# Optimization experiments

Measured on AMD Instinct MI355X. Metric: run time of the kernel, lower is better.

## Reference

```python
import jax, jax.numpy as jnp
import numpy as np

N = 6144
M_VID = 1024
M_AUD = 128
APPERTURE = 20
EPS = 1e-6


def setup_inputs() -> dict:
    key = jax.random.key(0)
    ks = jax.random.split(key, 16)
    s = 0.02
    inp = {
        "x": jax.random.normal(ks[0], (1, N, M_VID), dtype=jnp.float32),
        "x_audio": jax.random.normal(ks[1], (1, N, M_AUD), dtype=jnp.float32),
        "seq_len": N,
        "audio_len": N,
        # video self-attention (torch Linear convention: W is [out, in])
        "Wk_v": jax.random.normal(ks[2], (M_VID, M_VID), dtype=jnp.float32) * s,
        "Wq_v": jax.random.normal(ks[3], (M_VID, M_VID), dtype=jnp.float32) * s,
        "Wv_v": jax.random.normal(ks[4], (M_VID, M_VID), dtype=jnp.float32) * s,
        "Wo_v": jax.random.normal(ks[5], (M_VID, M_VID), dtype=jnp.float32) * s,
        # audio self-attention
        "Wk_a": jax.random.normal(ks[6], (M_AUD, M_AUD), dtype=jnp.float32) * s,
        "Wq_a": jax.random.normal(ks[7], (M_AUD, M_AUD), dtype=jnp.float32) * s,
        "Wv_a": jax.random.normal(ks[8], (M_AUD, M_AUD), dtype=jnp.float32) * s,
        "Wo_a": jax.random.normal(ks[9], (M_AUD, M_AUD), dtype=jnp.float32) * s,
        # MLP head
        "ka_w": jax.random.normal(ks[10], (1024, M_VID + M_AUD), dtype=jnp.float32) * s,
        "ka_b": jnp.zeros((1024,), dtype=jnp.float32),
        "kd_w": jax.random.normal(ks[11], (1, 1024), dtype=jnp.float32) * s,
        "kd_b": jnp.zeros((1,), dtype=jnp.float32),
        # layer norms
        "ln_y_g": jnp.ones((M_VID,), dtype=jnp.float32),
        "ln_y_b": jnp.zeros((M_VID,), dtype=jnp.float32),
        "ln_ya_g": jnp.ones((M_AUD,), dtype=jnp.float32),
        "ln_ya_b": jnp.zeros((M_AUD,), dtype=jnp.float32),
        "ln_ka_g": jnp.ones((1024,), dtype=jnp.float32),
        "ln_ka_b": jnp.zeros((1024,), dtype=jnp.float32),
    }
    return inp


def _layer_norm(x, g, b):
    mu = jnp.mean(x, axis=-1, keepdims=True)
    var = jnp.mean((x - mu) ** 2, axis=-1, keepdims=True)
    return (x - mu) / jnp.sqrt(var + EPS) * g + b


def _self_attention(x, Wk, Wq, Wv, Wo):
    # x: [N, d]
    n = x.shape[0]
    K = x @ Wk.T
    Q = (x @ Wq.T) * 0.06
    V = x @ Wv.T
    logits = Q @ K.T  # [N, N]
    # keep only |i-j| < apperture (trimask masks |i-j| >= apperture)
    idx = jnp.arange(n)
    band = jnp.abs(idx[:, None] - idx[None, :]) < APPERTURE
    logits = jnp.where(band, logits, -jnp.inf)
    att = jax.nn.softmax(logits, axis=-1)  # [N, N]
    # torch: y = (V^T @ att)^T == att^T @ V  (note the transpose on att!)
    y = att.T @ V
    return y @ Wo.T, att


def reference(x, x_audio, seq_len, audio_len,
              Wk_v, Wq_v, Wv_v, Wo_v,
              Wk_a, Wq_a, Wv_a, Wo_a,
              ka_w, ka_b, kd_w, kd_b,
              ln_y_g, ln_y_b, ln_ya_g, ln_ya_b, ln_ka_g, ln_ka_b):
    m = x.shape[2]
    m_audio = x_audio.shape[2]
    xf = x.reshape(-1, m)            # [N, 1024]
    xa = x_audio.reshape(-1, m_audio)  # [N, 128]

    y, att_w = _self_attention(xf, Wk_v, Wq_v, Wv_v, Wo_v)
    y = _layer_norm(y + xf, ln_y_g, ln_y_b)

    ya, att_wa = _self_attention(xa, Wk_a, Wq_a, Wv_a, Wo_a)
    ya = _layer_norm(ya + xa, ln_ya_g, ln_ya_b)

    y_comb = jnp.concatenate((y, ya), axis=1)        # [N, 1152]
    att_comb = jnp.concatenate((att_w, att_wa), axis=1)  # [N, 2N]

    h = jax.nn.relu(y_comb @ ka_w.T + ka_b)
    h = _layer_norm(h, ln_ka_g, ln_ka_b)
    score = jax.nn.sigmoid(h @ kd_w.T + kd_b)  # [N, 1]
    score = score.reshape(1, -1)               # [1, N]
    return score, att_comb
```

## Files before the change

kernel.cpp:

```cpp
#include <hip/hip_runtime.h>
#include <stdint.h>

typedef unsigned short u16;
typedef unsigned int u32;
typedef __attribute__((ext_vector_type(8))) short bf16x8;
typedef __attribute__((ext_vector_type(4))) short s16x4;
typedef __attribute__((ext_vector_type(4))) float f32x4;
typedef __attribute__((ext_vector_type(2))) float f32x2;

#define DEV __device__ __forceinline__

DEV u16 f2bf(float f) {
  union { float f; unsigned u; } v; v.f = f;
  unsigned r = v.u + 0x7fffu + ((v.u >> 16) & 1u);
  return (u16)(r >> 16);
}
DEV float bf2f(u16 h) {
  union { u32 u; float f; } v; v.u = ((u32)h) << 16; return v.f;
}
DEV float lo16(u32 w) { union { u32 u; float f; } v; v.u = w << 16; return v.f; }
DEV float hi16(u32 w) { union { u32 u; float f; } v; v.u = w & 0xFFFF0000u; return v.f; }
DEV int imax(int a, int b) { return a > b ? a : b; }
DEV int imin(int a, int b) { return a < b ? a : b; }

DEV int xcd_swz(int b0, int nwg) {
  int q = nwg >> 3, r = nwg & 7, x = b0 & 7, l = b0 >> 3;
  return (x < r ? x * (q + 1) : r * (q + 1) + (x - r) * q) + l;
}

DEV void g2lds16(const u16* g, u16* l) {
  __builtin_amdgcn_global_load_lds(
      (const __attribute__((address_space(1))) void*)g,
      (__attribute__((address_space(3))) void*)l, 16, 0, 0);
}

#define NSEG 5
struct CastTab {
  const float* src[NSEG];
  u16* dst[NSEG];
  int start[NSEG + 1];
};
struct TransTab {
  const float* src[6];
  u16* dst[6];
  int n[6];
  int start[7];
};

__global__ __launch_bounds__(256) void vas_prep(CastTab t, int total4,
                                                int castBlocks, TransTab tt) {
  if ((int)blockIdx.x < castBlocks) {
    int idx = blockIdx.x * 256 + threadIdx.x;
    if (idx >= total4) return;
    int s = 0;
#pragma unroll
    for (int k = 1; k < NSEG; ++k)
      if (idx >= t.start[k]) s = k;
    int local = idx - t.start[s];
    f32x4 f = ((const f32x4*)t.src[s])[local];
    s16x4 o;
    o.x = (short)f2bf(f.x);
    o.y = (short)f2bf(f.y);
    o.z = (short)f2bf(f.z);
    o.w = (short)f2bf(f.w);
    ((s16x4*)t.dst[s])[local] = o;
  } else {
    __shared__ float tl[32][33];
    int b = blockIdx.x - castBlocks;
    int s = 0;
#pragma unroll
    for (int k = 1; k < 6; ++k)
      if (b >= tt.start[k]) s = k;
    b -= tt.start[s];
    const float* src = tt.src[s];
    u16* dst = tt.dst[s];
    const int n = tt.n[s];
    const int tpr = n >> 5;
    const int tr = (b / tpr) * 32, tc = (b % tpr) * 32;
    const int lx = threadIdx.x & 31, ly = threadIdx.x >> 5;
#pragma unroll
    for (int r = 0; r < 4; ++r)
      tl[ly + r * 8][lx] = src[(size_t)(tr + ly + r * 8) * n + tc + lx];
    __syncthreads();
#pragma unroll
    for (int r = 0; r < 4; ++r)
      dst[(size_t)(tc + ly + r * 8) * n + tr + lx] = f2bf(tl[lx][ly + r * 8]);
  }
}

struct GemmP {
  const u16* A;
  const u16* W;
  void* C;
  const float* bias;
  int M, Nn, K, mode;
};

__global__ __launch_bounds__(256) void vas_gemm4(
    GemmP p0, GemmP p1, GemmP p2, GemmP p3, int s1, int s2, int s3) {
  const int bs = xcd_swz(blockIdx.x, gridDim.x);

  GemmP p;
  int bid;
  if (bs < s1) { p = p0; bid = bs; }
  else if (bs < s2) { p = p1; bid = bs - s1; }
  else if (bs < s3) { p = p2; bid = bs - s2; }
  else { p = p3; bid = bs - s3; }

  __shared__ u16 As[2][128 * 32];
  __shared__ u16 Ws[2][128 * 32];
  const int tid = threadIdx.x;
  const int lane = tid & 63;
  const int wave = tid >> 6;

  const int Mb = p.M >> 7, Nb = p.Nn >> 7;
  const int GM = 8;
  int per = GM * Nb;
  int g = bid / per;
  int rem = bid - g * per;
  int gm = imin(GM, Mb - g * GM);
  int mblk = g * GM + rem % gm;
  int nblk = rem / gm;
  const int m0 = mblk * 128;
  const int n0 = nblk * 128;
  const int wm = (wave >> 1) * 64;
  const int wn = (wave & 1) * 64;

  const int smat = wave >> 1;
  const int skh = wave & 1;
  const u16* ssrc = smat ? p.W : p.A;
  const int sbase = smat ? n0 : m0;
  u16* sdstBase = (smat ? &Ws[skh][0] : &As[skh][0]) + lane * 8;
  const int srow = lane >> 2;
  const int scol = (lane & 3) * 8;

  f32x4 acc[4][4] = {};

  for (int k0 = 0; k0 < p.K; k0 += 64) {
#pragma unroll
    for (int u = 0; u < 8; ++u) {
      int r0 = u * 16;
      g2lds16(ssrc + (size_t)(sbase + r0 + srow) * p.K + (k0 + skh * 32 + scol),
              sdstBase + r0 * 32);
    }
    __syncthreads();
#pragma unroll
    for (int kk = 0; kk < 2; ++kk) {
      bf16x8 af[4], bfr[4];
#pragma unroll
      for (int t = 0; t < 4; ++t)
        af[t] = *(const bf16x8*)(&As[kk][0] + (wm + t * 16 + (lane & 15)) * 32 + (lane >> 4) * 8);
#pragma unroll
      for (int t = 0; t < 4; ++t)
        bfr[t] = *(const bf16x8*)(&Ws[kk][0] + (wn + t * 16 + (lane & 15)) * 32 + (lane >> 4) * 8);
#pragma unroll
      for (int mi = 0; mi < 4; ++mi)
#pragma unroll
        for (int ni = 0; ni < 4; ++ni)
          acc[mi][ni] = __builtin_amdgcn_mfma_f32_16x16x32_bf16(af[mi], bfr[ni], acc[mi][ni], 0, 0, 0);
    }
    __syncthreads();
  }

#pragma unroll
  for (int mi = 0; mi < 4; ++mi) {
#pragma unroll
    for (int ni = 0; ni < 4; ++ni) {
      int col = n0 + wn + ni * 16 + (lane & 15);
      float bv = p.bias ? p.bias[col] : 0.f;
#pragma unroll
      for (int r = 0; r < 4; ++r) {
        int row = m0 + wm + mi * 16 + (lane >> 4) * 4 + r;
        float vv = acc[mi][ni][r] + bv;
        size_t idx = (size_t)row * p.Nn + col;
        if (p.mode == 0) ((float*)p.C)[idx] = vv;
        else if (p.mode == 1) ((u16*)p.C)[idx] = f2bf(fmaxf(vv, 0.f));
        else ((u16*)p.C)[idx] = f2bf(vv);
      }
    }
  }
}

__global__ __launch_bounds__(256) void vas_gemmh(
    GemmP p, const float* __restrict__ kw, const float* __restrict__ gw,
    float* __restrict__ part) {
  const int bid = xcd_swz(blockIdx.x, gridDim.x);

  __shared__ u16 As[2][128 * 32];
  __shared__ u16 Ws[2][128 * 32];
  __shared__ float hp[2][128][3];
  const int tid = threadIdx.x;
  const int lane = tid & 63;
  const int wave = tid >> 6;

  const int Mb = p.M >> 7, Nb = p.Nn >> 7;
  const int GM = 8;
  int per = GM * Nb;
  int g = bid / per;
  int rem = bid - g * per;
  int gm = imin(GM, Mb - g * GM);
  int mblk = g * GM + rem % gm;
  int nblk = rem / gm;
  const int m0 = mblk * 128;
  const int n0 = nblk * 128;
  const int wm = (wave >> 1) * 64;
  const int wn = (wave & 1) * 64;

  const int smat = wave >> 1;
  const int skh = wave & 1;
  const u16* ssrc = smat ? p.W : p.A;
  const int sbase = smat ? n0 : m0;
  u16* sdstBase = (smat ? &Ws[skh][0] : &As[skh][0]) + lane * 8;
  const int srow = lane >> 2;
  const int scol = (lane & 3) * 8;

  f32x4 acc[4][4] = {};

  for (int k0 = 0; k0 < p.K; k0 += 64) {
#pragma unroll
    for (int u = 0; u < 8; ++u) {
      int r0 = u * 16;
      g2lds16(ssrc + (size_t)(sbase + r0 + srow) * p.K + (k0 + skh * 32 + scol),
              sdstBase + r0 * 32);
    }
    __syncthreads();
#pragma unroll
    for (int kk = 0; kk < 2; ++kk) {
      bf16x8 af[4], bfr[4];
#pragma unroll
      for (int t = 0; t < 4; ++t)
        af[t] = *(const bf16x8*)(&As[kk][0] + (wm + t * 16 + (lane & 15)) * 32 + (lane >> 4) * 8);
#pragma unroll
      for (int t = 0; t < 4; ++t)
        bfr[t] = *(const bf16x8*)(&Ws[kk][0] + (wn + t * 16 + (lane & 15)) * 32 + (lane >> 4) * 8);
#pragma unroll
      for (int mi = 0; mi < 4; ++mi)
#pragma unroll
        for (int ni = 0; ni < 4; ++ni)
          acc[mi][ni] = __builtin_amdgcn_mfma_f32_16x16x32_bf16(af[mi], bfr[ni], acc[mi][ni], 0, 0, 0);
    }
    __syncthreads();
  }

  float kwg[4], bb[4];
#pragma unroll
  for (int ni = 0; ni < 4; ++ni) {
    int col = n0 + wn + ni * 16 + (lane & 15);
    kwg[ni] = kw[col] * gw[col];
    bb[ni] = p.bias ? p.bias[col] : 0.f;
  }
#pragma unroll
  for (int mi = 0; mi < 4; ++mi) {
#pragma unroll
    for (int r = 0; r < 4; ++r) {
      float s1 = 0.f, s2 = 0.f, dd = 0.f;
#pragma unroll
      for (int ni = 0; ni < 4; ++ni) {
        float vv = fmaxf(acc[mi][ni][r] + bb[ni], 0.f);
        s1 += vv;
        s2 += vv * vv;
        dd += vv * kwg[ni];
      }
#pragma unroll
      for (int off = 1; off < 16; off <<= 1) {
        s1 += __shfl_xor(s1, off);
        s2 += __shfl_xor(s2, off);
        dd += __shfl_xor(dd, off);
      }
      if ((lane & 15) == 0) {
        int row = wm + mi * 16 + (lane >> 4) * 4 + r;
        hp[wave & 1][row][0] = s1;
        hp[wave & 1][row][1] = s2;
        hp[wave & 1][row][2] = dd;
      }
    }
  }
  __syncthreads();
  if (tid < 128) {
    float* pp = part + ((size_t)(m0 + tid) * 8 + nblk) * 3;
    pp[0] = hp[0][tid][0] + hp[1][tid][0];
    pp[1] = hp[0][tid][1] + hp[1][tid][1];
    pp[2] = hp[0][tid][2] + hp[1][tid][2];
  }
}

__global__ __launch_bounds__(256) void vas_score(
    const float* __restrict__ part, const float* __restrict__ kw,
    const float* __restrict__ g, const float* __restrict__ b,
    const float* __restrict__ kb, float* __restrict__ score, int N) {
  const int tid = threadIdx.x, lane = tid & 63, wave = tid >> 6;
  __shared__ float shc[2][4];
  f32x4 kv = ((const f32x4*)kw)[tid];
  f32x4 gv = ((const f32x4*)g)[tid];
  f32x4 bv = ((const f32x4*)b)[tid];
  float c1 = kv.x * gv.x + kv.y * gv.y + kv.z * gv.z + kv.w * gv.w;
  float c2 = kv.x * bv.x + kv.y * bv.y + kv.z * bv.z + kv.w * bv.w;
#pragma unroll
  for (int off = 32; off; off >>= 1) {
    c1 += __shfl_xor(c1, off);
    c2 += __shfl_xor(c2, off);
  }
  if (lane == 0) { shc[0][wave] = c1; shc[1][wave] = c2; }
  __syncthreads();
  float C1 = shc[0][0] + shc[0][1] + shc[0][2] + shc[0][3];
  float C2 = shc[1][0] + shc[1][1] + shc[1][2] + shc[1][3];
  int row = blockIdx.x * 256 + tid;
  if (row < N) {
    const float* pp = part + (size_t)row * 24;
    float s1 = 0.f, s2 = 0.f, dd = 0.f;
#pragma unroll
    for (int k = 0; k < 8; ++k) {
      s1 += pp[k * 3];
      s2 += pp[k * 3 + 1];
      dd += pp[k * 3 + 2];
    }
    float mu = s1 / 1024.f;
    float var = s2 / 1024.f - mu * mu;
    float inv = rsqrtf(var + 1e-6f);
    float P = inv * dd - inv * mu * C1 + C2 + kb[0];
    score[row] = 1.f / (1.f + __expf(-P));
  }
}

__global__ __launch_bounds__(256) void vas_battn(
    const u16* __restrict__ Xv, const u16* __restrict__ Xa,
    const u16* __restrict__ KKVv, const u16* __restrict__ KKVa,
    float* __restrict__ bandV, float* __restrict__ bandA,
    float* __restrict__ attBase, int N, float scale, int vb) {
  const int lane = threadIdx.x & 63;
  const int wave = threadIdx.x >> 6;
  const bool video = blockIdx.x < (u32)vb;
  const int i = (video ? blockIdx.x : blockIdx.x - vb) * 4 + wave;
  const int lo = imax(i - 19, 0);
  const int hi = imin(i + 19, N - 1);
  const int nj = hi - lo + 1;
  float logit = 0.f;
  __shared__ float a_sh[4][40];

  if (video) {
    float qf[16];
    const u16* qrow = Xv + (size_t)i * 1024;
#pragma unroll
    for (int c = 0; c < 2; ++c) {
      bf16x8 qv = *(const bf16x8*)(qrow + c * 512 + lane * 8);
      const u32* qw = (const u32*)&qv;
#pragma unroll
      for (int t = 0; t < 4; ++t) {
        qf[c * 8 + 2 * t] = lo16(qw[t]);
        qf[c * 8 + 2 * t + 1] = hi16(qw[t]);
      }
    }
#pragma unroll 2
    for (int s = 0; s < nj; ++s) {
      const u16* kr = KKVv + (size_t)(lo + s) * 2048;
      float p = 0.f;
#pragma unroll
      for (int c = 0; c < 2; ++c) {
        bf16x8 kv = *(const bf16x8*)(kr + c * 512 + lane * 8);
        const u32* kw = (const u32*)&kv;
#pragma unroll
        for (int t = 0; t < 4; ++t)
          p += lo16(kw[t]) * qf[c * 8 + 2 * t] + hi16(kw[t]) * qf[c * 8 + 2 * t + 1];
      }
#pragma unroll
      for (int off = 32; off; off >>= 1) p += __shfl_xor(p, off);
      if (lane == s) logit = p;
    }
  } else {
    u32 q = *(const u32*)(Xa + (size_t)i * 128 + lane * 2);
    float q0 = lo16(q), q1 = hi16(q);
#pragma unroll 2
    for (int s = 0; s < nj; ++s) {
      u32 k = *(const u32*)(KKVa + (size_t)(lo + s) * 256 + lane * 2);
      float p = lo16(k) * q0 + hi16(k) * q1;
#pragma unroll
      for (int off = 32; off; off >>= 1) p += __shfl_xor(p, off);
      if (lane == s) logit = p;
    }
  }

  logit *= scale;
  float v = (lane < nj) ? logit : -3.4e38f;
  float mx = v;
#pragma unroll
  for (int off = 32; off; off >>= 1) mx = fmaxf(mx, __shfl_xor(mx, off));
  float e = (lane < nj) ? __expf(v - mx) : 0.f;
  float den = e;
#pragma unroll
  for (int off = 32; off; off >>= 1) den += __shfl_xor(den, off);
  float att = (lane < nj) ? e / den : 0.f;
  float* band = video ? bandV : bandA;
  if (lane < 40) {
    band[i * 40 + lane] = att;
    a_sh[wave][lane] = att;
  }

  f32x4* rowp = (f32x4*)(attBase + (size_t)i * 2 * N + (video ? 0 : N));
  const int nchunks = N / 4;
  const int cLo = lo >> 2, cHi = hi >> 2;
  for (int c = lane; c < nchunks; c += 64) {
    f32x4 o = {0.f, 0.f, 0.f, 0.f};
    if (c >= cLo && c <= cHi) {
      int col0 = c * 4;
#pragma unroll
      for (int e2 = 0; e2 < 4; ++e2) {
        int col = col0 + e2;
        if (col >= lo && col <= hi) o[e2] = a_sh[wave][col - lo];
      }
    }
    __builtin_nontemporal_store(o, &rowp[c]);
  }
}

#define JT 8
__global__ __launch_bounds__(256) void vas_apply_ln(
    const u16* __restrict__ KKVv, const u16* __restrict__ KKVa,
    const float* __restrict__ bandV, const float* __restrict__ bandA,
    const float* __restrict__ Xv, const float* __restrict__ Xa,
    const float* __restrict__ gv, const float* __restrict__ bv_,
    const float* __restrict__ ga, const float* __restrict__ ba,
    u16* __restrict__ out, int outStride, int N, int vb) {
  const int tid = threadIdx.x;
  __shared__ float a_sh[(JT + 38) * JT];
  __shared__ float red[2][JT][4];

  if (blockIdx.x < (u32)vb) {
    const int j0 = blockIdx.x * JT;
    const int base = j0 - 19;
    for (int idx = tid; idx < (JT + 38) * JT; idx += 256) {
      int s = idx / JT, jj = idx % JT;
      int i = base + s;
      int j = j0 + jj;
      float w = 0.f;
      if (i >= 0 && i < N) {
        int d = j - i;
        if (d > -20 && d < 20) w = bandV[i * 40 + (j - imax(i - 19, 0))];
      }
      a_sh[s * JT + jj] = w;
    }
    __syncthreads();

    f32x4 acc[JT] = {};
    const int sLo = imax(0, -base);
    const int sHi = imin(JT + 38, N - base);
    s16x4 nxt = *(const s16x4*)(KKVv + (size_t)(base + sLo) * 2048 + 1024 + tid * 4);
    for (int s = sLo; s < sHi; ++s) {
      s16x4 raw = nxt;
      if (s + 1 < sHi)
        nxt = *(const s16x4*)(KKVv + (size_t)(base + s + 1) * 2048 + 1024 + tid * 4);
      f32x4 vv;
      vv.x = bf2f((u16)raw.x);
      vv.y = bf2f((u16)raw.y);
      vv.z = bf2f((u16)raw.z);
      vv.w = bf2f((u16)raw.w);
#pragma unroll
      for (int jj = 0; jj < JT; ++jj) {
        float a = a_sh[s * JT + jj];
        acc[jj].x += a * vv.x;
        acc[jj].y += a * vv.y;
        acc[jj].z += a * vv.z;
        acc[jj].w += a * vv.w;
      }
    }

    const int lane = tid & 63, wave = tid >> 6;
#pragma unroll
    for (int jj = 0; jj < JT; ++jj) {
      f32x4 x4 = ((const f32x4*)(Xv + (size_t)(j0 + jj) * 1024))[tid];
      f32x4 v;
      v.x = acc[jj].x + x4.x;
      v.y = acc[jj].y + x4.y;
      v.z = acc[jj].z + x4.z;
      v.w = acc[jj].w + x4.w;
      acc[jj] = v;
      float s = v.x + v.y + v.z + v.w;
      float s2 = v.x * v.x + v.y * v.y + v.z * v.z + v.w * v.w;
#pragma unroll
      for (int off = 32; off; off >>= 1) {
        s += __shfl_xor(s, off);
        s2 += __shfl_xor(s2, off);
      }
      if (lane == 0) { red[0][jj][wave] = s; red[1][jj][wave] = s2; }
    }
    __syncthreads();
    f32x4 gg = ((const f32x4*)gv)[tid];
    f32x4 bb = ((const f32x4*)bv_)[tid];
#pragma unroll
    for (int jj = 0; jj < JT; ++jj) {
      float S = red[0][jj][0] + red[0][jj][1] + red[0][jj][2] + red[0][jj][3];
      float S2 = red[1][jj][0] + red[1][jj][1] + red[1][jj][2] + red[1][jj][3];
      float mu = S / 1024.f;
      float var = S2 / 1024.f - mu * mu;
      float inv = rsqrtf(var + 1e-6f);
      f32x4 v = acc[jj];
      s16x4 o;
      o.x = (short)f2bf((v.x - mu) * inv * gg.x + bb.x);
      o.y = (short)f2bf((v.y - mu) * inv * gg.y + bb.y);
      o.z = (short)f2bf((v.z - mu) * inv * gg.z + bb.z);
      o.w = (short)f2bf((v.w - mu) * inv * gg.w + bb.w);
      *(s16x4*)(out + (size_t)(j0 + jj) * outStride + tid * 4) = o;
    }
  } else {
    const int lane = tid & 63;
    const int wave = tid >> 6;
    const int j = (blockIdx.x - vb) * 4 + wave;
    const int lo = imax(j - 19, 0);
    const int hi = imin(j + 19, N - 1);
    const int ni = hi - lo + 1;
    float* aw = a_sh + wave * 40;
    if (lane < ni) {
      int i = lo + lane;
      aw[lane] = bandA[i * 40 + (j - imax(i - 19, 0))];
    }
    __syncthreads();
    f32x2 acc = {0.f, 0.f};
#pragma unroll 4
    for (int s = 0; s < ni; ++s) {
      float a = aw[s];
      u32 k = *(const u32*)(KKVa + (size_t)(lo + s) * 256 + 128 + lane * 2);
      acc.x += a * lo16(k);
      acc.y += a * hi16(k);
    }
    f32x2 x2 = *(const f32x2*)(Xa + (size_t)j * 128 + lane * 2);
    float vx = acc.x + x2.x;
    float vy = acc.y + x2.y;
    float s = vx + vy, s2 = vx * vx + vy * vy;
#pragma unroll
    for (int off = 32; off; off >>= 1) {
      s += __shfl_xor(s, off);
      s2 += __shfl_xor(s2, off);
    }
    float mu = s / 128.f;
    float var = s2 / 128.f - mu * mu;
    float inv = rsqrtf(var + 1e-6f);
    f32x2 g2 = *(const f32x2*)(ga + lane * 2);
    f32x2 b2 = *(const f32x2*)(ba + lane * 2);
    u32 o = (u32)f2bf((vx - mu) * inv * g2.x + b2.x) |
            ((u32)f2bf((vy - mu) * inv * g2.y + b2.y) << 16);
    *(u32*)(out + (size_t)j * outStride + 1024 + lane * 2) = o;
  }
}

extern "C" void kernel_launch(void* const* d_in, const int* in_sizes, int n_in,
                              void* d_out, int out_size, void* d_ws, size_t ws_size,
                              hipStream_t stream) {
  const float* x = (const float*)d_in[0];
  const float* xa = (const float*)d_in[1];
  const float* Wk_v = (const float*)d_in[4];
  const float* Wq_v = (const float*)d_in[5];
  const float* Wv_v = (const float*)d_in[6];
  const float* Wo_v = (const float*)d_in[7];
  const float* Wk_a = (const float*)d_in[8];
  const float* Wq_a = (const float*)d_in[9];
  const float* Wv_a = (const float*)d_in[10];
  const float* Wo_a = (const float*)d_in[11];
  const float* ka_w = (const float*)d_in[12];
  const float* ka_b = (const float*)d_in[13];
  const float* kd_w = (const float*)d_in[14];
  const float* kd_b = (const float*)d_in[15];
  const float* ln_y_g = (const float*)d_in[16];
  const float* ln_y_b = (const float*)d_in[17];
  const float* ln_ya_g = (const float*)d_in[18];
  const float* ln_ya_b = (const float*)d_in[19];
  const float* ln_ka_g = (const float*)d_in[20];
  const float* ln_ka_b = (const float*)d_in[21];

  const int N = in_sizes[0] / 1024;
  const int MV = 1024, MA = 128, MH = 1152;

  char* wsb = (char*)d_ws;
  size_t off = 0;
  auto alloc = [&](size_t bytes) -> void* {
    void* p = wsb + off;
    off += (bytes + 255) & ~(size_t)255;
    return p;
  };
  u16* xf_b   = (u16*)alloc((size_t)N * MV * 2);
  u16* xa_b   = (u16*)alloc((size_t)N * MA * 2);
  u16* wov_b  = (u16*)alloc((size_t)MV * MV * 2);
  u16* woa_b  = (u16*)alloc((size_t)MA * MA * 2);
  u16* wqTv   = (u16*)alloc((size_t)MV * MV * 2);
  u16* wkTv   = (u16*)alloc((size_t)MV * MV * 2);
  u16* wvTv   = (u16*)alloc((size_t)MV * MV * 2);
  u16* wqTa   = (u16*)alloc((size_t)MA * MA * 2);
  u16* wkTa   = (u16*)alloc((size_t)MA * MA * 2);
  u16* wvTa   = (u16*)alloc((size_t)MA * MA * 2);
  u16* wWv    = (u16*)alloc((size_t)2 * MV * MV * 2);
  u16* wWa    = (u16*)alloc((size_t)2 * MA * MA * 2);
  u16* kaw_b  = (u16*)alloc((size_t)1024 * MH * 2);
  u16* KKVv   = (u16*)alloc((size_t)N * 2 * MV * 2);
  u16* KKVa   = (u16*)alloc((size_t)N * 2 * MA * 2);
  float* bandV = (float*)alloc((size_t)N * 40 * 4);
  float* bandA = (float*)alloc((size_t)N * 40 * 4);
  u16* ycomb_b = (u16*)alloc((size_t)N * MH * 2);
  float* part_b = (float*)alloc((size_t)N * 8 * 3 * 4);

  float* dout = (float*)d_out;
  float* attBase = dout + N;

  {
    CastTab t;
    int c = 0, cum = 0;
    auto seg = [&](const float* s, u16* d, size_t n) {
      t.src[c] = s; t.dst[c] = d; t.start[c] = cum; cum += (int)(n / 4); ++c;
    };
    seg(x, xf_b, (size_t)N * MV);
    seg(xa, xa_b, (size_t)N * MA);
    seg(Wo_v, wov_b, (size_t)MV * MV);
    seg(Wo_a, woa_b, (size_t)MA * MA);
    seg(ka_w, kaw_b, (size_t)1024 * MH);
    t.start[c] = cum;
    int castBlocks = (cum + 255) / 256;

    TransTab tt;
    int c2 = 0, cum2 = 0;
    auto seg2 = [&](const float* s, u16* d, int n) {
      tt.src[c2] = s; tt.dst[c2] = d; tt.n[c2] = n; tt.start[c2] = cum2;
      cum2 += (n / 32) * (n / 32); ++c2;
    };
    seg2(Wq_v, wqTv, MV);
    seg2(Wk_v, wkTv, MV);
    seg2(Wv_v, wvTv, MV);
    seg2(Wq_a, wqTa, MA);
    seg2(Wk_a, wkTa, MA);
    seg2(Wv_a, wvTa, MA);
    tt.start[c2] = cum2;

    vas_prep<<<castBlocks + cum2, 256, 0, stream>>>(t, cum, castBlocks, tt);
  }

  {
    GemmP gv = {wqTv, wkTv, wWv, nullptr, MV, MV, MV, 2};
    GemmP uv = {wov_b, wvTv, wWv + (size_t)MV * MV, nullptr, MV, MV, MV, 2};
    GemmP ga = {wqTa, wkTa, wWa, nullptr, MA, MA, MA, 2};
    GemmP ua = {woa_b, wvTa, wWa + (size_t)MA * MA, nullptr, MA, MA, MA, 2};
    int bg = (MV / 128) * (MV / 128);
    vas_gemm4<<<2 * bg + 2, 256, 0, stream>>>(gv, uv, ga, ua, bg, 2 * bg, 2 * bg + 1);
  }

  {
    GemmP pv = {xf_b, wWv, KKVv, nullptr, N, 2 * MV, MV, 2};
    GemmP pa = {xa_b, wWa, KKVa, nullptr, N, 2 * MA, MA, 2};
    int bv = (N / 128) * (2 * MV / 128);
    int ba = (N / 128) * (2 * MA / 128);
    vas_gemm4<<<bv + ba, 256, 0, stream>>>(pv, pa, pa, pa, bv, bv + ba, bv + ba);
  }

  vas_battn<<<N / 2, 256, 0, stream>>>(xf_b, xa_b, KKVv, KKVa, bandV, bandA,
                                       attBase, N, 0.06f, N / 4);

  vas_apply_ln<<<N / JT + N / 4, 256, 0, stream>>>(
      KKVv, KKVa, bandV, bandA, x, xa,
      ln_y_g, ln_y_b, ln_ya_g, ln_ya_b, ycomb_b, MH, N, N / JT);

  {
    GemmP ph = {ycomb_b, kaw_b, nullptr, ka_b, N, 1024, MH, 1};
    int bh = (N / 128) * (1024 / 128);
    vas_gemmh<<<bh, 256, 0, stream>>>(ph, kd_w, ln_ka_g, part_b);
  }

  vas_score<<<(N + 255) / 256, 256, 0, stream>>>(
      part_b, kd_w, ln_ka_g, ln_ka_b, kd_b, dout, N);
}
```

Before: 551.1 us.

## Move dense attention-matrix writes into MLP-head GEMM launch to overlap with compute

The band-attention kernel now only writes the compact 40-wide band weights, and the full zero-padded N x 2N attention matrix is written by extra blocks appended to the head GEMM launch. The goal is to overlap the large bandwidth-bound store with the compute-bound GEMM and to shorten the attention kernel. The writer blocks inherit the GEMM kernel's shared-memory footprint, which may limit their occupancy, and overlap depends on block scheduling order.

```diff
diff --git a/kernel.cpp b/kernel.cpp
--- a/kernel.cpp
+++ b/kernel.cpp
@@ -183,13 +183,47 @@
 
 __global__ __launch_bounds__(256) void vas_gemmh(
     GemmP p, const float* __restrict__ kw, const float* __restrict__ gw,
-    float* __restrict__ part) {
-  const int bid = xcd_swz(blockIdx.x, gridDim.x);
+    float* __restrict__ part, int bh,
+    const float* __restrict__ bandV, const float* __restrict__ bandA,
+    float* __restrict__ attBase, int N) {
+  const int tid = threadIdx.x;
+
+  if ((int)blockIdx.x >= bh) {
+    const int i = blockIdx.x - bh;
+    __shared__ float bw[80];
+    const int lo = imax(i - 19, 0);
+    const int hi = imin(i + 19, N - 1);
+    if (tid < 40) bw[tid] = bandV[i * 40 + tid];
+    else if (tid < 80) bw[tid] = bandA[i * 40 + (tid - 40)];
+    __syncthreads();
+    const int nch = N / 4;
+    const int cLo = lo >> 2, cHi = hi >> 2;
+    f32x4* rowp = (f32x4*)(attBase + (size_t)i * 2 * N);
+#pragma unroll 1
+    for (int half = 0; half < 2; ++half) {
+      const float* w = bw + half * 40;
+      f32x4* rp = rowp + half * nch;
+      for (int c = tid; c < nch; c += 256) {
+        f32x4 o = {0.f, 0.f, 0.f, 0.f};
+        if (c >= cLo && c <= cHi) {
+          int col0 = c * 4;
+#pragma unroll
+          for (int e2 = 0; e2 < 4; ++e2) {
+            int col = col0 + e2;
+            if (col >= lo && col <= hi) o[e2] = w[col - lo];
+          }
+        }
+        __builtin_nontemporal_store(o, &rp[c]);
+      }
+    }
+    return;
+  }
+
+  const int bid = xcd_swz(blockIdx.x, bh);
 
   __shared__ u16 As[2][128 * 32];
   __shared__ u16 Ws[2][128 * 32];
   __shared__ float hp[2][128][3];
-  const int tid = threadIdx.x;
   const int lane = tid & 63;
   const int wave = tid >> 6;
 
@@ -326,7 +360,7 @@
     const u16* __restrict__ Xv, const u16* __restrict__ Xa,
     const u16* __restrict__ KKVv, const u16* __restrict__ KKVa,
     float* __restrict__ bandV, float* __restrict__ bandA,
-    float* __restrict__ attBase, int N, float scale, int vb) {
+    int N, float scale, int vb) {
   const int lane = threadIdx.x & 63;
   const int wave = threadIdx.x >> 6;
   const bool video = blockIdx.x < (u32)vb;
@@ -335,7 +369,6 @@
   const int hi = imin(i + 19, N - 1);
   const int nj = hi - lo + 1;
   float logit = 0.f;
-  __shared__ float a_sh[4][40];
 
   if (video) {
     float qf[16];
@@ -390,26 +423,7 @@
   for (int off = 32; off; off >>= 1) den += __shfl_xor(den, off);
   float att = (lane < nj) ? e / den : 0.f;
   float* band = video ? bandV : bandA;
-  if (lane < 40) {
-    band[i * 40 + lane] = att;
-    a_sh[wave][lane] = att;
-  }
-
-  f32x4* rowp = (f32x4*)(attBase + (size_t)i * 2 * N + (video ? 0 : N));
-  const int nchunks = N / 4;
-  const int cLo = lo >> 2, cHi = hi >> 2;
-  for (int c = lane; c < nchunks; c += 64) {
-    f32x4 o = {0.f, 0.f, 0.f, 0.f};
-    if (c >= cLo && c <= cHi) {
-      int col0 = c * 4;
-#pragma unroll
-      for (int e2 = 0; e2 < 4; ++e2) {
-        int col = col0 + e2;
-        if (col >= lo && col <= hi) o[e2] = a_sh[wave][col - lo];
-      }
-    }
-    __builtin_nontemporal_store(o, &rowp[c]);
-  }
+  if (lane < 40) band[i * 40 + lane] = att;
 }
 
 #define JT 8
@@ -647,7 +661,7 @@
   }
 
   vas_battn<<<N / 2, 256, 0, stream>>>(xf_b, xa_b, KKVv, KKVa, bandV, bandA,
-                                       attBase, N, 0.06f, N / 4);
+                                       N, 0.06f, N / 4);
 
   vas_apply_ln<<<N / JT + N / 4, 256, 0, stream>>>(
       KKVv, KKVa, bandV, bandA, x, xa,
@@ -656,7 +670,8 @@
   {
     GemmP ph = {ycomb_b, kaw_b, nullptr, ka_b, N, 1024, MH, 1};
     int bh = (N / 128) * (1024 / 128);
-    vas_gemmh<<<bh, 256, 0, stream>>>(ph, kd_w, ln_ka_g, part_b);
+    vas_gemmh<<<bh + N, 256, 0, stream>>>(ph, kd_w, ln_ka_g, part_b, bh,
+                                          bandV, bandA, attBase, N);
   }
 
   vas_score<<<(N + 255) / 256, 256, 0, stream>>>(
```

New measurement: 529.5 us. 3.9% less time.
